# Optimization experiments

Hardware: AMD Instinct MI355X
Metric: run time of the kernel (lower is better)

## Reference

```python
import jax, jax.numpy as jnp
import numpy as np

N_NODES = 100000
N_EDGES = 1000000
F_IN = 256
HEADS = 2
C_OUT = 64
NEG_SLOPE = 0.2


def setup_inputs() -> dict:
    key = jax.random.key(0)
    k_x, k_e, k_ws, k_wd, k_a = jax.random.split(key, 5)
    x = jax.random.normal(k_x, (N_NODES, F_IN), dtype=jnp.float32)
    edge_index = jax.random.randint(k_e, (2, N_EDGES), 0, N_NODES, dtype=jnp.int64)
    # uniform init as in init_randoms('uniform'), scale is irrelevant for correctness
    W_src = jax.random.uniform(k_ws, (F_IN, HEADS * C_OUT), dtype=jnp.float32, minval=-0.1, maxval=0.1)
    W_dst = jax.random.uniform(k_wd, (F_IN, HEADS * C_OUT), dtype=jnp.float32, minval=-0.1, maxval=0.1)
    att = jax.random.uniform(k_a, (HEADS, C_OUT), dtype=jnp.float32, minval=-0.1, maxval=0.1)
    bias = jnp.zeros((HEADS * C_OUT,), dtype=jnp.float32)
    return {"x": x, "edge_index": edge_index, "W_src": W_src, "W_dst": W_dst, "att": att, "bias": bias}


def reference(x, edge_index, W_src, W_dst, att, bias):
    # GATv2 conv (MyGATConv), concat=True, add_self_loops=False, dropout=0
    N = x.shape[0]
    H, C = att.shape
    x_src = (x @ W_src).reshape(N, H, C)  # Theta_s x  [N,H,C]
    x_dst = (x @ W_dst).reshape(N, H, C)  # Theta_d x  [N,H,C]
    src = edge_index[0]  # j (source)
    dst = edge_index[1]  # i (target) -> segment index

    xj = x_src[src]                                   # [E,H,C]
    e = jax.nn.leaky_relu(xj + x_dst[dst], NEG_SLOPE)  # [E,H,C]
    logits = jnp.einsum('ehc,hc->eh', e, att)          # [E,H]

    # segment softmax over destination neighborhoods
    seg_max = jax.ops.segment_max(logits, dst, num_segments=N)  # [N,H]
    seg_max = jnp.where(jnp.isfinite(seg_max), seg_max, 0.0)
    ex = jnp.exp(logits - seg_max[dst])                # [E,H]
    denom = jax.ops.segment_sum(ex, dst, num_segments=N)  # [N,H]
    alpha = ex / (denom[dst] + 1e-16)                  # [E,H]

    # scatter-add aggregation of alpha * Theta_s x_j
    out = jax.ops.segment_sum(alpha[:, :, None] * xj, dst, num_segments=N)  # [N,H,C]
    return out.reshape(N, H * C) + bias
```

## Files before the change

### kernel.cpp

```cpp
#include <hip/hip_runtime.h>

#define F_IN 256
#define HC   128

typedef __attribute__((ext_vector_type(8))) short bf16x8;
typedef __attribute__((ext_vector_type(4))) float f32x4;

__device__ __forceinline__ unsigned short f2b(float f) {
    unsigned int u = __float_as_uint(f);
    return (unsigned short)((u + 0x7FFFu + ((u >> 16) & 1u)) >> 16);
}

__device__ __forceinline__ unsigned int f2b_pk(float lo, float hi) {
    unsigned int ul = __float_as_uint(lo);
    unsigned int uh = __float_as_uint(hi);
    ul = ul + 0x7FFFu + ((ul >> 16) & 1u);
    uh = uh + 0x7FFFu + ((uh >> 16) & 1u);
    return __builtin_amdgcn_perm(uh, ul, 0x07060302);
}

#define DPP_ADD(x, ctrl) \
    x += __int_as_float(__builtin_amdgcn_update_dpp(0, __float_as_int(x), ctrl, 0xF, 0xF, true))

__device__ __forceinline__ float row_sum16(float x) {
    DPP_ADD(x, 0xB1);
    DPP_ADD(x, 0x4E);
    DPP_ADD(x, 0x141);
    DPP_ADD(x, 0x140);
    return x;
}

__global__ __launch_bounds__(256) void k_prep(const float* __restrict__ Ws,
                                              const float* __restrict__ Wd,
                                              unsigned short* __restrict__ PB) {
    int tid = blockIdx.x * 256 + threadIdx.x;
    int nt  = tid >> 9;
    int rem = tid & 511;
    int t   = rem >> 6;
    int l   = rem & 63;
    int m   = l & 15;
    int w   = nt >> 2;
    int g   = nt & 3;
    int pos = w * 64 + m * 4 + g;
    int kbase = 32 * t + (l >> 4) * 8;

    const float* W;
    int n;
    if (pos < 128) {
        W = Ws; n = (pos & 1) * 64 + (pos >> 1);
    } else {
        int p2 = pos - 128;
        W = Wd; n = (p2 & 1) * 64 + (p2 >> 1);
    }
    union { bf16x8 v; unsigned short u[8]; } o;
#pragma unroll
    for (int j = 0; j < 8; ++j)
        o.u[j] = f2b(W[(kbase + j) * HC + n]);
    *(bf16x8*)(PB + (size_t)tid * 8) = o.v;
}

#define LIST_BLOCKS 1024
__global__ __launch_bounds__(256) void k_gemm_list(const float* __restrict__ x,
                                                   const unsigned short* __restrict__ PB,
                                                   unsigned short* __restrict__ xsrc_pk,
                                                   unsigned short* __restrict__ xdst_pk, int N,
                                                   const int* __restrict__ src,
                                                   const int* __restrict__ dst, int E,
                                                   int* __restrict__ head4,
                                                   uint2* __restrict__ rec) {
    if (blockIdx.x < LIST_BLOCKS) {
        int i = blockIdx.x * 256 + threadIdx.x;
        int stride = LIST_BLOCKS * 256;
        for (; i < E; i += stride) {
            int d = dst[i];
            int s = src[i];
            int old = atomicExch(&head4[(size_t)d * 4 + (i & 3)], i);
            rec[i] = make_uint2((unsigned int)old, (unsigned int)s);
        }
        return;
    }

    __shared__ unsigned short smem[64 * F_IN];
    char* sb = (char*)smem;

    const int wave = threadIdx.x >> 6;
    const int lane = threadIdx.x & 63;
    const int m = lane & 15;
    const int q = lane >> 4;
    const long row0 = (long)(blockIdx.x - LIST_BLOCKS) * 64;

    {
        const int col = lane * 4;
        const int wbyte_base = col * 2;
#pragma unroll 8
        for (int i = 0; i < 16; ++i) {
            int row = i * 4 + wave;
            long grow = row0 + row;
            if (grow >= N) grow = N - 1;
            float4 a = *(const float4*)(x + grow * F_IN + col);
            uint2 v;
            v.x = f2b_pk(a.x, a.y);
            v.y = f2b_pk(a.z, a.w);
            *(uint2*)(sb + row * 512 + (wbyte_base ^ ((row & 7) << 4))) = v;
        }
    }
    __syncthreads();

    f32x4 acc[4][4];
#pragma unroll
    for (int a = 0; a < 4; ++a)
#pragma unroll
        for (int b = 0; b < 4; ++b) acc[a][b] = (f32x4){0.f, 0.f, 0.f, 0.f};

#pragma unroll
    for (int t = 0; t < 8; ++t) {
        const int bytein = t * 64 + q * 16;
        bf16x8 af[4];
#pragma unroll
        for (int mt = 0; mt < 4; ++mt) {
            const int row = mt * 16 + m;
            af[mt] = *(const bf16x8*)(sb + row * 512 + (bytein ^ ((row & 7) << 4)));
        }
#pragma unroll
        for (int g = 0; g < 4; ++g) {
            const int nt = wave * 4 + g;
            bf16x8 bf = *(const bf16x8*)(PB + ((size_t)(nt * 8 + t) * 64 + lane) * 8);
#pragma unroll
            for (int mt = 0; mt < 4; ++mt)
                acc[mt][g] = __builtin_amdgcn_mfma_f32_16x16x32_bf16(af[mt], bf, acc[mt][g], 0, 0, 0);
        }
    }

    unsigned short* dstArr = (wave < 2) ? xsrc_pk : xdst_pk;
    const int colOff = ((wave & 1) * 64) + m * 4;
#pragma unroll
    for (int mt = 0; mt < 4; ++mt) {
#pragma unroll
        for (int r = 0; r < 4; ++r) {
            long row = row0 + mt * 16 + q * 4 + r;
            if (row >= N) continue;
            uint2 v;
            v.x = f2b_pk(acc[mt][0][r], acc[mt][1][r]);
            v.y = f2b_pk(acc[mt][2][r], acc[mt][3][r]);
            *(uint2*)(dstArr + row * HC + colOff) = v;
        }
    }
}

__global__ __launch_bounds__(256) void k_agg(const unsigned int* __restrict__ xsrc_u,
                                             const unsigned int* __restrict__ xdst_u,
                                             const int* __restrict__ head4,
                                             const uint2* __restrict__ rec,
                                             const float* __restrict__ att,
                                             const float* __restrict__ bias,
                                             float* __restrict__ out, int N) {
    int wid  = threadIdx.x >> 6;
    int lane = threadIdx.x & 63;
    int node = blockIdx.x * 4 + wid;
    if (node >= N) return;
    int g = lane >> 4;
    int s = lane & 15;

    uint4 D = *(const uint4*)(xdst_u + (size_t)node * 64 + s * 4);
    float xd0[4], xd1[4];
    {
        unsigned int du[4] = {D.x, D.y, D.z, D.w};
#pragma unroll
        for (int k = 0; k < 4; ++k) {
            xd0[k] = __uint_as_float(du[k] << 16);
            xd1[k] = __uint_as_float(du[k] & 0xFFFF0000u);
        }
    }
    float4 A0 = *(const float4*)(att + s * 4);
    float4 A1 = *(const float4*)(att + 64 + s * 4);
    float c10[4] = {0.6f * A0.x, 0.6f * A0.y, 0.6f * A0.z, 0.6f * A0.w};
    float c20[4] = {0.4f * A0.x, 0.4f * A0.y, 0.4f * A0.z, 0.4f * A0.w};
    float c11[4] = {0.6f * A1.x, 0.6f * A1.y, 0.6f * A1.z, 0.6f * A1.w};
    float c21[4] = {0.4f * A1.x, 0.4f * A1.y, 0.4f * A1.z, 0.4f * A1.w};

    float l0 = 0.f, l1 = 0.f;
    float o0[4] = {0.f, 0.f, 0.f, 0.f}, o1[4] = {0.f, 0.f, 0.f, 0.f};

    int e = head4[(size_t)node * 4 + g];
    uint2 r;
    if (e >= 0) r = rec[e];
    while (__any(e >= 0)) {
        if (e >= 0) {
            int j = (int)r.y;
            uint4 U = *(const uint4*)(xsrc_u + (size_t)j * 64 + s * 4);
            int en = (int)r.x;
            if (en >= 0) r = rec[en];
            unsigned int cu[4] = {U.x, U.y, U.z, U.w};
            float xj0[4], xj1[4];
            float s0 = 0.f, s1 = 0.f;
#pragma unroll
            for (int k = 0; k < 4; ++k) {
                xj0[k] = __uint_as_float(cu[k] << 16);
                xj1[k] = __uint_as_float(cu[k] & 0xFFFF0000u);
                float e0 = xj0[k] + xd0[k];
                float e1 = xj1[k] + xd1[k];
                s0 = fmaf(c10[k], e0, s0); s0 = fmaf(c20[k], fabsf(e0), s0);
                s1 = fmaf(c11[k], e1, s1); s1 = fmaf(c21[k], fabsf(e1), s1);
            }
            s0 = row_sum16(s0);
            s1 = row_sum16(s1);
            float w0 = __expf(s0);
            float w1 = __expf(s1);
            l0 += w0; l1 += w1;
#pragma unroll
            for (int k = 0; k < 4; ++k) {
                o0[k] = fmaf(w0, xj0[k], o0[k]);
                o1[k] = fmaf(w1, xj1[k], o1[k]);
            }
            e = en;
        }
    }

#define XRED(v) { v += __shfl_xor(v, 16, 64); v += __shfl_xor(v, 32, 64); }
    XRED(l0); XRED(l1);
#pragma unroll
    for (int k = 0; k < 4; ++k) { XRED(o0[k]); XRED(o1[k]); }
#undef XRED

    if (g == 0) {
        float inv0 = __builtin_amdgcn_rcpf(l0 + 1e-16f);
        float inv1 = __builtin_amdgcn_rcpf(l1 + 1e-16f);
        float4 B0 = *(const float4*)(bias + s * 4);
        float4 B1 = *(const float4*)(bias + 64 + s * 4);
        float4 R0 = {o0[0] * inv0 + B0.x, o0[1] * inv0 + B0.y,
                     o0[2] * inv0 + B0.z, o0[3] * inv0 + B0.w};
        float4 R1 = {o1[0] * inv1 + B1.x, o1[1] * inv1 + B1.y,
                     o1[2] * inv1 + B1.z, o1[3] * inv1 + B1.w};
        *(float4*)(out + (size_t)node * HC + s * 4) = R0;
        *(float4*)(out + (size_t)node * HC + 64 + s * 4) = R1;
    }
}

extern "C" void kernel_launch(void* const* d_in, const int* in_sizes, int n_in,
                              void* d_out, int out_size, void* d_ws, size_t ws_size,
                              hipStream_t stream) {
    const float* x    = (const float*)d_in[0];
    const int*   ei   = (const int*)d_in[1];
    const float* Ws   = (const float*)d_in[2];
    const float* Wd   = (const float*)d_in[3];
    const float* att  = (const float*)d_in[4];
    const float* bias = (const float*)d_in[5];
    float* out = (float*)d_out;

    const int N = in_sizes[0] / F_IN;
    const int E = in_sizes[1] / 2;
    const int* src = ei;
    const int* dst = ei + E;

    char* ws = (char*)d_ws;
    size_t off = 0;
    auto alloc = [&](size_t bytes) -> char* {
        off = (off + 255) & ~(size_t)255;
        char* p = ws + off;
        off += bytes;
        return p;
    };
    unsigned short* xsrc_pk = (unsigned short*)alloc((size_t)N * HC * sizeof(unsigned short));
    unsigned short* xdst_pk = (unsigned short*)alloc((size_t)N * HC * sizeof(unsigned short));
    unsigned short* PB = (unsigned short*)alloc(256 * 256 * sizeof(unsigned short));
    int*   head4 = (int*)alloc((size_t)N * 4 * sizeof(int));
    uint2* rec   = (uint2*)alloc((size_t)E * sizeof(uint2));

    hipMemsetAsync(head4, 0xFF, (size_t)N * 4 * sizeof(int), stream);

    k_prep<<<32, 256, 0, stream>>>(Ws, Wd, PB);
    k_gemm_list<<<LIST_BLOCKS + (int)((N + 63) / 64), 256, 0, stream>>>(
        x, PB, xsrc_pk, xdst_pk, N, src, dst, E, head4, rec);
    k_agg<<<(N + 3) / 4, 256, 0, stream>>>((const unsigned int*)xsrc_pk,
                                           (const unsigned int*)xdst_pk,
                                           head4, rec, att, bias, out, N);
}
```

Measured before the change: 290.5 us.

## Replace per-destination linked lists with bounded bucket arrays plus overflow list

Edge bucketing now uses an atomic counter per destination and writes source indices into a fixed array of up to 32 slots per node, falling back to a single linked list only for overflow edges. The aggregation kernel reads these contiguous slots and software-pipelines the source-row gathers three deep, replacing the serial pointer chase through records. This is meant to remove dependent-load latency in the linked-list traversal. In exchange it uses more workspace, needs an extra memset, and issues padding gathers of row 0 for invalid slots.

```diff
diff --git a/kernel.cpp b/kernel.cpp
--- a/kernel.cpp
+++ b/kernel.cpp
@@ -2,6 +2,7 @@
 
 #define F_IN 256
 #define HC   128
+#define KMAX 32
 
 typedef __attribute__((ext_vector_type(8))) short bf16x8;
 typedef __attribute__((ext_vector_type(4))) float f32x4;
@@ -66,7 +67,9 @@
                                                    unsigned short* __restrict__ xdst_pk, int N,
                                                    const int* __restrict__ src,
                                                    const int* __restrict__ dst, int E,
-                                                   int* __restrict__ head4,
+                                                   int* __restrict__ cnt,
+                                                   int* __restrict__ eidx,
+                                                   int* __restrict__ head1,
                                                    uint2* __restrict__ rec) {
     if (blockIdx.x < LIST_BLOCKS) {
         int i = blockIdx.x * 256 + threadIdx.x;
@@ -74,8 +77,13 @@
         for (; i < E; i += stride) {
             int d = dst[i];
             int s = src[i];
-            int old = atomicExch(&head4[(size_t)d * 4 + (i & 3)], i);
-            rec[i] = make_uint2((unsigned int)old, (unsigned int)s);
+            int slot = atomicAdd(&cnt[d], 1);
+            if (slot < KMAX) {
+                eidx[(size_t)d * KMAX + slot] = s;
+            } else {
+                int old = atomicExch(&head1[d], i);
+                rec[i] = make_uint2((unsigned int)old, (unsigned int)s);
+            }
         }
         return;
     }
@@ -149,7 +157,9 @@
 
 __global__ __launch_bounds__(256) void k_agg(const unsigned int* __restrict__ xsrc_u,
                                              const unsigned int* __restrict__ xdst_u,
-                                             const int* __restrict__ head4,
+                                             const int* __restrict__ cnt,
+                                             const int* __restrict__ eidx,
+                                             const int* __restrict__ head1,
                                              const uint2* __restrict__ rec,
                                              const float* __restrict__ att,
                                              const float* __restrict__ bias,
@@ -181,38 +191,82 @@
     float l0 = 0.f, l1 = 0.f;
     float o0[4] = {0.f, 0.f, 0.f, 0.f}, o1[4] = {0.f, 0.f, 0.f, 0.f};
 
-    int e = head4[(size_t)node * 4 + g];
-    uint2 r;
-    if (e >= 0) r = rec[e];
-    while (__any(e >= 0)) {
-        if (e >= 0) {
-            int j = (int)r.y;
-            uint4 U = *(const uint4*)(xsrc_u + (size_t)j * 64 + s * 4);
-            int en = (int)r.x;
-            if (en >= 0) r = rec[en];
-            unsigned int cu[4] = {U.x, U.y, U.z, U.w};
-            float xj0[4], xj1[4];
-            float s0 = 0.f, s1 = 0.f;
-#pragma unroll
-            for (int k = 0; k < 4; ++k) {
-                xj0[k] = __uint_as_float(cu[k] << 16);
-                xj1[k] = __uint_as_float(cu[k] & 0xFFFF0000u);
-                float e0 = xj0[k] + xd0[k];
-                float e1 = xj1[k] + xd1[k];
-                s0 = fmaf(c10[k], e0, s0); s0 = fmaf(c20[k], fabsf(e0), s0);
-                s1 = fmaf(c11[k], e1, s1); s1 = fmaf(c21[k], fabsf(e1), s1);
+    const int degT = cnt[node];
+    const int deg  = degT < KMAX ? degT : KMAX;
+    const int* base = eidx + (size_t)node * KMAX;
+
+    int t = g;
+    int v0 = t < deg; int j0 = v0 ? base[t] : 0; t += 4;
+    int v1 = t < deg; int j1 = v1 ? base[t] : 0; t += 4;
+    int v2 = t < deg; int j2 = v2 ? base[t] : 0; t += 4;
+    uint4 U0 = *(const uint4*)(xsrc_u + (size_t)j0 * 64 + s * 4);
+    uint4 U1 = *(const uint4*)(xsrc_u + (size_t)j1 * 64 + s * 4);
+
+    while (__any(v0)) {
+        uint4 U2 = *(const uint4*)(xsrc_u + (size_t)j2 * 64 + s * 4);
+        int v3 = t < deg; int j3 = v3 ? base[t] : 0; t += 4;
+
+        unsigned int cu[4] = {U0.x, U0.y, U0.z, U0.w};
+        float xj0[4], xj1[4];
+        float s0 = 0.f, s1 = 0.f;
+#pragma unroll
+        for (int k = 0; k < 4; ++k) {
+            xj0[k] = __uint_as_float(cu[k] << 16);
+            xj1[k] = __uint_as_float(cu[k] & 0xFFFF0000u);
+            float e0 = xj0[k] + xd0[k];
+            float e1 = xj1[k] + xd1[k];
+            s0 = fmaf(c10[k], e0, s0); s0 = fmaf(c20[k], fabsf(e0), s0);
+            s1 = fmaf(c11[k], e1, s1); s1 = fmaf(c21[k], fabsf(e1), s1);
+        }
+        s0 = row_sum16(s0);
+        s1 = row_sum16(s1);
+        float w0 = v0 ? __expf(s0) : 0.f;
+        float w1 = v0 ? __expf(s1) : 0.f;
+        l0 += w0; l1 += w1;
+#pragma unroll
+        for (int k = 0; k < 4; ++k) {
+            o0[k] = fmaf(w0, xj0[k], o0[k]);
+            o1[k] = fmaf(w1, xj1[k], o1[k]);
+        }
+        v0 = v1; j0 = j1; U0 = U1;
+        v1 = v2; j1 = j2; U1 = U2;
+        v2 = v3; j2 = j3;
+    }
+
+    if (degT > KMAX) {
+        int e = (g == 0) ? head1[node] : -1;
+        uint2 r;
+        if (e >= 0) r = rec[e];
+        while (__any(e >= 0)) {
+            if (e >= 0) {
+                int j = (int)r.y;
+                uint4 U = *(const uint4*)(xsrc_u + (size_t)j * 64 + s * 4);
+                int en = (int)r.x;
+                if (en >= 0) r = rec[en];
+                unsigned int cu[4] = {U.x, U.y, U.z, U.w};
+                float xj0[4], xj1[4];
+                float s0 = 0.f, s1 = 0.f;
+#pragma unroll
+                for (int k = 0; k < 4; ++k) {
+                    xj0[k] = __uint_as_float(cu[k] << 16);
+                    xj1[k] = __uint_as_float(cu[k] & 0xFFFF0000u);
+                    float e0 = xj0[k] + xd0[k];
+                    float e1 = xj1[k] + xd1[k];
+                    s0 = fmaf(c10[k], e0, s0); s0 = fmaf(c20[k], fabsf(e0), s0);
+                    s1 = fmaf(c11[k], e1, s1); s1 = fmaf(c21[k], fabsf(e1), s1);
+                }
+                s0 = row_sum16(s0);
+                s1 = row_sum16(s1);
+                float w0 = __expf(s0);
+                float w1 = __expf(s1);
+                l0 += w0; l1 += w1;
+#pragma unroll
+                for (int k = 0; k < 4; ++k) {
+                    o0[k] = fmaf(w0, xj0[k], o0[k]);
+                    o1[k] = fmaf(w1, xj1[k], o1[k]);
+                }
+                e = en;
             }
-            s0 = row_sum16(s0);
-            s1 = row_sum16(s1);
-            float w0 = __expf(s0);
-            float w1 = __expf(s1);
-            l0 += w0; l1 += w1;
-#pragma unroll
-            for (int k = 0; k < 4; ++k) {
-                o0[k] = fmaf(w0, xj0[k], o0[k]);
-                o1[k] = fmaf(w1, xj1[k], o1[k]);
-            }
-            e = en;
         }
     }
 
@@ -263,15 +317,18 @@
     unsigned short* xsrc_pk = (unsigned short*)alloc((size_t)N * HC * sizeof(unsigned short));
     unsigned short* xdst_pk = (unsigned short*)alloc((size_t)N * HC * sizeof(unsigned short));
     unsigned short* PB = (unsigned short*)alloc(256 * 256 * sizeof(unsigned short));
-    int*   head4 = (int*)alloc((size_t)N * 4 * sizeof(int));
+    int*   cnt   = (int*)alloc((size_t)N * sizeof(int));
+    int*   head1 = (int*)alloc((size_t)N * sizeof(int));
+    int*   eidx  = (int*)alloc((size_t)N * KMAX * sizeof(int));
     uint2* rec   = (uint2*)alloc((size_t)E * sizeof(uint2));
 
-    hipMemsetAsync(head4, 0xFF, (size_t)N * 4 * sizeof(int), stream);
+    hipMemsetAsync(cnt, 0, (size_t)N * sizeof(int), stream);
+    hipMemsetAsync(head1, 0xFF, (size_t)N * sizeof(int), stream);
 
     k_prep<<<32, 256, 0, stream>>>(Ws, Wd, PB);
     k_gemm_list<<<LIST_BLOCKS + (int)((N + 63) / 64), 256, 0, stream>>>(
-        x, PB, xsrc_pk, xdst_pk, N, src, dst, E, head4, rec);
+        x, PB, xsrc_pk, xdst_pk, N, src, dst, E, cnt, eidx, head1, rec);
     k_agg<<<(N + 3) / 4, 256, 0, stream>>>((const unsigned int*)xsrc_pk,
                                            (const unsigned int*)xdst_pk,
-                                           head4, rec, att, bias, out, N);
-}
+                                           cnt, eidx, head1, rec, att, bias, out, N);
+}
```

Measured after the change: 313.4 us. 1.08x slower.

## Map one 16-lane group per node with single linked list and prefetch

Applied to the files above, without the earlier changes.

Replaces the four interleaved per-node edge lists with a single head per node. Each 16-lane quarter-wave now walks a whole node's list, so a 256-thread block covers 16 nodes and the final cross-group shuffle reduction goes away. The next record and the next source row are prefetched before the current edge is processed, overlapping the dependent loads of the linked-list walk. Leaky ReLU becomes max(e, 0.2e) using packed float2 math. The trade-off is longer serial chains per group, since average degree is about 10, plus more divergence between nodes in a wave and more atomic contention on the single head.

```diff
diff --git a/kernel.cpp b/kernel.cpp
--- a/kernel.cpp
+++ b/kernel.cpp
@@ -5,6 +5,7 @@
 
 typedef __attribute__((ext_vector_type(8))) short bf16x8;
 typedef __attribute__((ext_vector_type(4))) float f32x4;
+typedef __attribute__((ext_vector_type(2))) float f32x2;
 
 __device__ __forceinline__ unsigned short f2b(float f) {
     unsigned int u = __float_as_uint(f);
@@ -22,12 +23,12 @@
 #define DPP_ADD(x, ctrl) \
     x += __int_as_float(__builtin_amdgcn_update_dpp(0, __float_as_int(x), ctrl, 0xF, 0xF, true))
 
-__device__ __forceinline__ float row_sum16(float x) {
-    DPP_ADD(x, 0xB1);
-    DPP_ADD(x, 0x4E);
-    DPP_ADD(x, 0x141);
-    DPP_ADD(x, 0x140);
-    return x;
+__device__ __forceinline__ f32x2 row_sum16_2(f32x2 v) {
+    DPP_ADD(v.x, 0xB1);  DPP_ADD(v.y, 0xB1);
+    DPP_ADD(v.x, 0x4E);  DPP_ADD(v.y, 0x4E);
+    DPP_ADD(v.x, 0x141); DPP_ADD(v.y, 0x141);
+    DPP_ADD(v.x, 0x140); DPP_ADD(v.y, 0x140);
+    return v;
 }
 
 __global__ __launch_bounds__(256) void k_prep(const float* __restrict__ Ws,
@@ -66,7 +67,7 @@
                                                    unsigned short* __restrict__ xdst_pk, int N,
                                                    const int* __restrict__ src,
                                                    const int* __restrict__ dst, int E,
-                                                   int* __restrict__ head4,
+                                                   int* __restrict__ head1,
                                                    uint2* __restrict__ rec) {
     if (blockIdx.x < LIST_BLOCKS) {
         int i = blockIdx.x * 256 + threadIdx.x;
@@ -74,7 +75,7 @@
         for (; i < E; i += stride) {
             int d = dst[i];
             int s = src[i];
-            int old = atomicExch(&head4[(size_t)d * 4 + (i & 3)], i);
+            int old = atomicExch(&head1[d], i);
             rec[i] = make_uint2((unsigned int)old, (unsigned int)s);
         }
         return;
@@ -149,88 +150,87 @@
 
 __global__ __launch_bounds__(256) void k_agg(const unsigned int* __restrict__ xsrc_u,
                                              const unsigned int* __restrict__ xdst_u,
-                                             const int* __restrict__ head4,
+                                             const int* __restrict__ head1,
                                              const uint2* __restrict__ rec,
                                              const float* __restrict__ att,
                                              const float* __restrict__ bias,
                                              float* __restrict__ out, int N) {
-    int wid  = threadIdx.x >> 6;
-    int lane = threadIdx.x & 63;
-    int node = blockIdx.x * 4 + wid;
-    if (node >= N) return;
-    int g = lane >> 4;
-    int s = lane & 15;
-
-    uint4 D = *(const uint4*)(xdst_u + (size_t)node * 64 + s * 4);
-    float xd0[4], xd1[4];
+    const int lane = threadIdx.x & 63;
+    const int s = lane & 15;
+    const int node = blockIdx.x * 16 + (threadIdx.x >> 4);
+    const bool vn = node < N;
+    const int nc = vn ? node : 0;
+
+    uint4 D = *(const uint4*)(xdst_u + (size_t)nc * 64 + s * 4);
+    f32x2 xd[4], at[4];
     {
         unsigned int du[4] = {D.x, D.y, D.z, D.w};
 #pragma unroll
-        for (int k = 0; k < 4; ++k) {
-            xd0[k] = __uint_as_float(du[k] << 16);
-            xd1[k] = __uint_as_float(du[k] & 0xFFFF0000u);
-        }
-    }
-    float4 A0 = *(const float4*)(att + s * 4);
-    float4 A1 = *(const float4*)(att + 64 + s * 4);
-    float c10[4] = {0.6f * A0.x, 0.6f * A0.y, 0.6f * A0.z, 0.6f * A0.w};
-    float c20[4] = {0.4f * A0.x, 0.4f * A0.y, 0.4f * A0.z, 0.4f * A0.w};
-    float c11[4] = {0.6f * A1.x, 0.6f * A1.y, 0.6f * A1.z, 0.6f * A1.w};
-    float c21[4] = {0.4f * A1.x, 0.4f * A1.y, 0.4f * A1.z, 0.4f * A1.w};
-
-    float l0 = 0.f, l1 = 0.f;
-    float o0[4] = {0.f, 0.f, 0.f, 0.f}, o1[4] = {0.f, 0.f, 0.f, 0.f};
-
-    int e = head4[(size_t)node * 4 + g];
-    uint2 r;
-    if (e >= 0) r = rec[e];
+        for (int k = 0; k < 4; ++k)
+            xd[k] = (f32x2){__uint_as_float(du[k] << 16),
+                            __uint_as_float(du[k] & 0xFFFF0000u)};
+    }
+    {
+        float4 A0 = *(const float4*)(att + s * 4);
+        float4 A1 = *(const float4*)(att + 64 + s * 4);
+        at[0] = (f32x2){A0.x, A1.x}; at[1] = (f32x2){A0.y, A1.y};
+        at[2] = (f32x2){A0.z, A1.z}; at[3] = (f32x2){A0.w, A1.w};
+    }
+
+    f32x2 l2 = (f32x2){0.f, 0.f};
+    f32x2 o2[4];
+#pragma unroll
+    for (int k = 0; k < 4; ++k) o2[k] = (f32x2){0.f, 0.f};
+
+    int e = vn ? head1[nc] : -1;
+    uint2 r = rec[e >= 0 ? e : 0];
+    int j = (e >= 0) ? (int)r.y : 0;
+    uint4 U = *(const uint4*)(xsrc_u + (size_t)j * 64 + s * 4);
+
     while (__any(e >= 0)) {
         if (e >= 0) {
-            int j = (int)r.y;
-            uint4 U = *(const uint4*)(xsrc_u + (size_t)j * 64 + s * 4);
             int en = (int)r.x;
-            if (en >= 0) r = rec[en];
+            uint2 rn = rec[en >= 0 ? en : 0];
+
             unsigned int cu[4] = {U.x, U.y, U.z, U.w};
-            float xj0[4], xj1[4];
-            float s0 = 0.f, s1 = 0.f;
+            f32x2 xj[4];
+            f32x2 s2 = (f32x2){0.f, 0.f};
 #pragma unroll
             for (int k = 0; k < 4; ++k) {
-                xj0[k] = __uint_as_float(cu[k] << 16);
-                xj1[k] = __uint_as_float(cu[k] & 0xFFFF0000u);
-                float e0 = xj0[k] + xd0[k];
-                float e1 = xj1[k] + xd1[k];
-                s0 = fmaf(c10[k], e0, s0); s0 = fmaf(c20[k], fabsf(e0), s0);
-                s1 = fmaf(c11[k], e1, s1); s1 = fmaf(c21[k], fabsf(e1), s1);
+                xj[k] = (f32x2){__uint_as_float(cu[k] << 16),
+                                __uint_as_float(cu[k] & 0xFFFF0000u)};
+                f32x2 e2 = xj[k] + xd[k];
+                f32x2 e5 = e2 * 0.2f;
+                f32x2 le;
+                le.x = fmaxf(e2.x, e5.x);
+                le.y = fmaxf(e2.y, e5.y);
+                s2 += at[k] * le;
             }
-            s0 = row_sum16(s0);
-            s1 = row_sum16(s1);
-            float w0 = __expf(s0);
-            float w1 = __expf(s1);
-            l0 += w0; l1 += w1;
-#pragma unroll
-            for (int k = 0; k < 4; ++k) {
-                o0[k] = fmaf(w0, xj0[k], o0[k]);
-                o1[k] = fmaf(w1, xj1[k], o1[k]);
-            }
-            e = en;
-        }
-    }
-
-#define XRED(v) { v += __shfl_xor(v, 16, 64); v += __shfl_xor(v, 32, 64); }
-    XRED(l0); XRED(l1);
-#pragma unroll
-    for (int k = 0; k < 4; ++k) { XRED(o0[k]); XRED(o1[k]); }
-#undef XRED
-
-    if (g == 0) {
-        float inv0 = __builtin_amdgcn_rcpf(l0 + 1e-16f);
-        float inv1 = __builtin_amdgcn_rcpf(l1 + 1e-16f);
+
+            int jn = (en >= 0) ? (int)rn.y : 0;
+            uint4 Un = *(const uint4*)(xsrc_u + (size_t)jn * 64 + s * 4);
+
+            s2 = row_sum16_2(s2);
+            f32x2 w2;
+            w2.x = __expf(s2.x);
+            w2.y = __expf(s2.y);
+            l2 += w2;
+#pragma unroll
+            for (int k = 0; k < 4; ++k) o2[k] += w2 * xj[k];
+
+            e = en; r = rn; U = Un;
+        }
+    }
+
+    if (vn) {
+        float inv0 = __builtin_amdgcn_rcpf(l2.x + 1e-16f);
+        float inv1 = __builtin_amdgcn_rcpf(l2.y + 1e-16f);
         float4 B0 = *(const float4*)(bias + s * 4);
         float4 B1 = *(const float4*)(bias + 64 + s * 4);
-        float4 R0 = {o0[0] * inv0 + B0.x, o0[1] * inv0 + B0.y,
-                     o0[2] * inv0 + B0.z, o0[3] * inv0 + B0.w};
-        float4 R1 = {o1[0] * inv1 + B1.x, o1[1] * inv1 + B1.y,
-                     o1[2] * inv1 + B1.z, o1[3] * inv1 + B1.w};
+        float4 R0 = {o2[0].x * inv0 + B0.x, o2[1].x * inv0 + B0.y,
+                     o2[2].x * inv0 + B0.z, o2[3].x * inv0 + B0.w};
+        float4 R1 = {o2[0].y * inv1 + B1.x, o2[1].y * inv1 + B1.y,
+                     o2[2].y * inv1 + B1.z, o2[3].y * inv1 + B1.w};
         *(float4*)(out + (size_t)node * HC + s * 4) = R0;
         *(float4*)(out + (size_t)node * HC + 64 + s * 4) = R1;
     }
@@ -263,15 +263,15 @@
     unsigned short* xsrc_pk = (unsigned short*)alloc((size_t)N * HC * sizeof(unsigned short));
     unsigned short* xdst_pk = (unsigned short*)alloc((size_t)N * HC * sizeof(unsigned short));
     unsigned short* PB = (unsigned short*)alloc(256 * 256 * sizeof(unsigned short));
-    int*   head4 = (int*)alloc((size_t)N * 4 * sizeof(int));
+    int*   head1 = (int*)alloc((size_t)N * sizeof(int));
     uint2* rec   = (uint2*)alloc((size_t)E * sizeof(uint2));
 
-    hipMemsetAsync(head4, 0xFF, (size_t)N * 4 * sizeof(int), stream);
+    hipMemsetAsync(head1, 0xFF, (size_t)N * sizeof(int), stream);
 
     k_prep<<<32, 256, 0, stream>>>(Ws, Wd, PB);
     k_gemm_list<<<LIST_BLOCKS + (int)((N + 63) / 64), 256, 0, stream>>>(
-        x, PB, xsrc_pk, xdst_pk, N, src, dst, E, head4, rec);
-    k_agg<<<(N + 3) / 4, 256, 0, stream>>>((const unsigned int*)xsrc_pk,
-                                           (const unsigned int*)xdst_pk,
-                                           head4, rec, att, bias, out, N);
-}
+        x, PB, xsrc_pk, xdst_pk, N, src, dst, E, head1, rec);
+    k_agg<<<(N + 15) / 16, 256, 0, stream>>>((const unsigned int*)xsrc_pk,
+                                             (const unsigned int*)xdst_pk,
+                                             head1, rec, att, bias, out, N);
+}
```

New measurement: 286.1 us. Within noise of the previous version (-1.5%).
